# Kernel optimization log

Measured on AMD Instinct MI355X. Metric: run time of the kernel, lower is better.

Reference implementation:

```python
import jax, jax.numpy as jnp
from jax import lax
import numpy as np

B, H, W = 8, 36, 100  # stride-8 feature map of 288x800 input
PAD = 4               # ms_ks // 2 for ms_ks = 9
EPS = 1e-5
FC_IN = 5 * (800 // 16) * (288 // 16)  # 4500


def setup_inputs() -> dict:
    key = jax.random.key(0)
    ks = jax.random.split(key, 12)
    r = lambda k, s, sc: jax.random.normal(k, s, jnp.float32) * sc
    return {
        "x": jax.random.normal(ks[0], (B, 512, H, W), jnp.float32),
        "w1a": r(ks[1], (1024, 512, 3, 3), 0.02),
        "bn1_g": jnp.ones(1024, jnp.float32), "bn1_b": jnp.zeros(1024, jnp.float32),
        "bn1_m": jnp.zeros(1024, jnp.float32), "bn1_v": jnp.ones(1024, jnp.float32),
        "w1b": r(ks[2], (128, 1024, 1, 1), 0.03),
        "bn2_g": jnp.ones(128, jnp.float32), "bn2_b": jnp.zeros(128, jnp.float32),
        "bn2_m": jnp.zeros(128, jnp.float32), "bn2_v": jnp.ones(128, jnp.float32),
        "w_ud": r(ks[3], (128, 128, 9), 0.02),
        "w_du": r(ks[4], (128, 128, 9), 0.02),
        "w_lr": r(ks[5], (128, 128, 9), 0.02),
        "w_rl": r(ks[6], (128, 128, 9), 0.02),
        "w2": r(ks[7], (5, 128, 1, 1), 0.05), "b2": jnp.zeros(5, jnp.float32),
        "fc1_w": r(ks[8], (128, FC_IN), 0.02), "fc1_b": jnp.zeros(128, jnp.float32),
        "fc2_w": r(ks[9], (4, 128), 0.05), "fc2_b": jnp.zeros(4, jnp.float32),
    }


def bn(x, g, b, m, v):
    s = (g / jnp.sqrt(v + EPS))
    return x * s[None, :, None, None] + (b - m * s)[None, :, None, None]


def conv2d(x, w, padding, dilation=(1, 1)):
    return lax.conv_general_dilated(x, w, (1, 1), padding, rhs_dilation=dilation,
                                    dimension_numbers=("NCHW", "OIHW", "NCHW"))


def conv1d(x, w):  # x [B,C,L], w [O,I,K]
    return lax.conv_general_dilated(x, w, (1,), [(PAD, PAD)],
                                    dimension_numbers=("NCH", "OIH", "NCH"))


def message_pass(x, w, axis, reverse):
    # x [B,C,H,W]; scan over `axis`, 1D conv along the other spatial dim
    xs = jnp.moveaxis(x, axis, 0)  # [L, B, C, other]
    if reverse:
        xs = xs[::-1]

    def step(prev, cur):
        new = cur + jax.nn.relu(conv1d(prev, w))
        return new, new

    first = xs[0]
    _, rest = lax.scan(step, first, xs[1:])
    out = jnp.concatenate([first[None], rest], axis=0)
    if reverse:
        out = out[::-1]
    return jnp.moveaxis(out, 0, axis)


def upsample_bilinear_ac(x, scale):
    # align_corners=True bilinear, NCHW
    b, c, h, w = x.shape
    ho, wo = h * scale, w * scale

    def grid(n_in, n_out):
        pos = jnp.arange(n_out, dtype=x.dtype) * ((n_in - 1) / (n_out - 1))
        i0 = jnp.clip(jnp.floor(pos).astype(jnp.int32), 0, n_in - 2)
        return i0, pos - i0.astype(x.dtype)

    i0, fh = grid(h, ho)
    j0, fw = grid(w, wo)
    xh = x[:, :, i0, :] * (1 - fh)[None, None, :, None] + x[:, :, i0 + 1, :] * fh[None, None, :, None]
    return xh[:, :, :, j0] * (1 - fw)[None, None, None, :] + xh[:, :, :, j0 + 1] * fw[None, None, None, :]


def reference(x, w1a, bn1_g, bn1_b, bn1_m, bn1_v, w1b, bn2_g, bn2_b, bn2_m, bn2_v,
              w_ud, w_du, w_lr, w_rl, w2, b2, fc1_w, fc1_b, fc2_w, fc2_b):
    # layer1: dilated 3x3 (pad=4, dil=4) -> BN -> ReLU -> 1x1 -> BN -> ReLU
    h = jax.nn.relu(bn(conv2d(x, w1a, [(4, 4), (4, 4)], dilation=(4, 4)), bn1_g, bn1_b, bn1_m, bn1_v))
    h = jax.nn.relu(bn(conv2d(h, w1b, [(0, 0), (0, 0)]), bn2_g, bn2_b, bn2_m, bn2_v))
    # message passing: up-down, down-up (vertical), left-right, right-left (horizontal)
    h = message_pass(h, w_ud, axis=2, reverse=False)
    h = message_pass(h, w_du, axis=2, reverse=True)
    h = message_pass(h, w_lr, axis=3, reverse=False)
    h = message_pass(h, w_rl, axis=3, reverse=True)
    # layer2 (Dropout2d is identity at eval): 1x1 conv -> 5 channels
    h = conv2d(h, w2, [(0, 0), (0, 0)]) + b2[None, :, None, None]
    seg_pred = upsample_bilinear_ac(h, 8)  # [B,5,288,800]
    # layer3: softmax over channels, then AvgPool2d(2,2)
    p = jax.nn.softmax(h, axis=1)
    b_, c_, hh, ww = p.shape
    p = p.reshape(b_, c_, hh // 2, 2, ww // 2, 2).mean(axis=(3, 5))
    # fc: flatten -> 128 -> ReLU -> 4 -> Sigmoid
    f = p.reshape(b_, -1)
    f = jax.nn.relu(f @ fc1_w.T + fc1_b)
    exist_pred = jax.nn.sigmoid(f @ fc2_w.T + fc2_b)
    return seg_pred, exist_pred
```

## Files before the change

kernel.cpp:

```cpp
#include <hip/hip_runtime.h>
#include <hip/hip_bf16.h>
#include <stdint.h>

typedef __bf16 bf16;
typedef bf16 bf16x8 __attribute__((ext_vector_type(8)));
typedef bf16 bf16x4 __attribute__((ext_vector_type(4)));
typedef float f32x4 __attribute__((ext_vector_type(4)));

#define NB 8
#define NH 36
#define NW 100
#define YS 44
#define XSZ 108
#define PIX 28800

#define AS1 __attribute__((address_space(1)))
#define AS3 __attribute__((address_space(3)))

__device__ __forceinline__ void g2l16(const bf16* g, bf16* l) {
    __builtin_amdgcn_global_load_lds((const AS1 void*)g, (AS3 void*)l, 16, 0, 0);
}

static constexpr size_t OFF_XP = 0;
static constexpr size_t SZ_XP  = (size_t)NB*YS*XSZ*512*2;
static constexpr size_t OFF_HP = OFF_XP + SZ_XP;
static constexpr size_t SZ_HP  = (size_t)NB*YS*XSZ*128*2;
static constexpr size_t OFF_A1 = OFF_HP + SZ_HP;
static constexpr size_t SZ_A1  = (size_t)1024*4608*2;
static constexpr size_t OFF_A2 = OFF_A1 + SZ_A1;
static constexpr size_t SZ_A2  = (size_t)128*1024*2;
static constexpr size_t OFF_AW = OFF_A2 + SZ_A2;
static constexpr size_t SZ_AW  = (size_t)4*9*128*128*2;
static constexpr size_t OFF_H1 = OFF_AW + SZ_AW;
static constexpr size_t SZ_H1  = (size_t)PIX*1024*2;
static constexpr size_t OFF_S1 = OFF_H1 + SZ_H1;
static constexpr size_t OFF_T1 = OFF_S1 + 4096;
static constexpr size_t OFF_S2 = OFF_T1 + 4096;
static constexpr size_t OFF_T2 = OFF_S2 + 512;
static constexpr size_t OFF_H5 = OFF_T2 + 512;
static constexpr size_t SZ_H5  = (size_t)NB*5*3600*4;
static constexpr size_t OFF_P  = OFF_H5 + SZ_H5;
static constexpr size_t OFF_F  = OFF_P + SZ_H5;
static constexpr size_t OFF_G  = OFF_F + 144128;

__global__ __launch_bounds__(256) void zero_k(uint4* __restrict__ p, int n) {
    int i = blockIdx.x * 256 + threadIdx.x;
    if (i < n) p[i] = uint4{0u, 0u, 0u, 0u};
}

__global__ __launch_bounds__(256) void prep_x(const float* __restrict__ x, bf16* __restrict__ xp) {
    int bid = blockIdx.x;
    int xc = bid & 3;  int r = bid >> 2;
    int cc = r & 15;   r >>= 4;
    int yo = r % 36;   int b = r / 36;
    int ci0 = cc * 32, xo0 = xc * 32;
    int wdt = 100 - xo0; if (wdt > 32) wdt = 32;
    __shared__ bf16 T[32 * 33];
    int t = threadIdx.x;
    int cl = t >> 5, xl = t & 31;
    if (xl < wdt) {
#pragma unroll
        for (int i = 0; i < 4; i++) {
            int ci = ci0 + cl + 8 * i;
            T[(cl + 8 * i) * 33 + xl] = (bf16)x[((size_t)(b * 512 + ci) * 36 + yo) * 100 + xo0 + xl];
        }
    }
    __syncthreads();
    if (t < 128) {
        int xo2 = t >> 2, oct = t & 3;
        if (xo2 < wdt) {
            bf16x8 vv;
#pragma unroll
            for (int j = 0; j < 8; j++) vv[j] = T[(oct * 8 + j) * 33 + xo2];
            *(bf16x8*)(xp + ((size_t)((b * YS + yo + 4) * XSZ) + xo0 + xo2 + 4) * 512 + ci0 + oct * 8) = vv;
        }
    }
}

__global__ __launch_bounds__(256) void prep_w1a(const float* __restrict__ w, bf16* __restrict__ A) {
    int co = blockIdx.x;
    __shared__ bf16 Wl[4608];
    const float* src = w + (size_t)co * 4608;
    for (int v = threadIdx.x; v < 4608; v += 256) Wl[v] = (bf16)src[v];
    __syncthreads();
    bf16* dst = A + (size_t)co * 4608;
    for (int v = threadIdx.x; v < 4608; v += 256) {
        int rr = v >> 9, ci = v & 511;
        dst[v] = Wl[ci * 9 + rr];
    }
}

__global__ __launch_bounds__(256) void prep_w1b(const float* __restrict__ w, bf16* __restrict__ A) {
    int i = blockIdx.x * 256 + threadIdx.x;
    if (i < 131072) A[i] = (bf16)w[i];
}

__global__ __launch_bounds__(256) void prep_msg(const float* __restrict__ w0, const float* __restrict__ w1,
                                                const float* __restrict__ w2m, const float* __restrict__ w3,
                                                bf16* __restrict__ Aw) {
    int idx = blockIdx.x * 256 + threadIdx.x;
    if (idx >= 4 * 147456) return;
    int w = idx / 147456, r = idx % 147456;
    int t9 = r / 16384, r2 = r % 16384;
    int co = r2 >> 7, ci = r2 & 127;
    const float* s = (w == 0) ? w0 : (w == 1) ? w1 : (w == 2) ? w2m : w3;
    Aw[idx] = (bf16)s[(co * 128 + ci) * 9 + t9];
}

__global__ __launch_bounds__(256) void prep_bn(const float* g1, const float* b1, const float* m1, const float* v1,
                                               const float* g2, const float* b2i, const float* m2, const float* v2,
                                               float* s1, float* t1, float* s2, float* t2) {
    int i = blockIdx.x * 256 + threadIdx.x;
    if (i < 1024) {
        float s = g1[i] / sqrtf(v1[i] + 1e-5f);
        s1[i] = s; t1[i] = b1[i] - m1[i] * s;
    } else if (i < 1152) {
        int c = i - 1024;
        float s = g2[c] / sqrtf(v2[c] + 1e-5f);
        s2[c] = s; t2[c] = b2i[c] - m2[c] * s;
    }
}

__device__ __forceinline__ void c1_koff(int ch, int& k0, int& xoff) {
    int ky = ch / 48, rem = ch - ky * 48;
    int kx = rem >> 4, c0 = (rem & 15) << 5;
    k0 = (ky * 3 + kx) * 512 + c0;
    xoff = (ky * XSZ + kx) * 2048 + c0;
}

__device__ __forceinline__ bf16x8 lds_frag(const bf16* S, int row, int q) {
    return *(const bf16x8*)(S + row * 32 + (((q ^ (row >> 1)) & 3) * 8));
}

__global__ __launch_bounds__(256) void conv1_gemm(const bf16* __restrict__ A, const bf16* __restrict__ xp,
                                                  const float* __restrict__ s1, const float* __restrict__ t1,
                                                  bf16* __restrict__ h1) {
    __shared__ __align__(16) bf16 SH[17408];
    bf16* As = SH;
    bf16* Bs = SH + 4096;
    const int t = threadIdx.x;
    const int pt = blockIdx.x, ct = blockIdx.y;
    const int co0 = ct * 128, p0 = pt * 128;
    const int wid = t >> 6, lane = t & 63;

    int aOff[2], bOff[2], ldsOff[2];
#pragma unroll
    for (int j = 0; j < 2; j++) {
        int p = wid * 128 + j * 64 + lane;
        int row = p >> 2;
        int oc = (p & 3) ^ ((p >> 3) & 3);
        aOff[j] = (co0 + row) * 4608 + oc * 8;
        int px = p0 + row;
        int b = px / 3600, rr = px % 3600;
        int y = rr / 100, xx = rr % 100;
        bOff[j] = ((b * YS + y) * XSZ + xx) * 512 + oc * 8;
        ldsOff[j] = (wid * 128 + j * 64) * 8;
    }

    const int mbase = (wid & 1) * 64, nbase = (wid >> 1) * 64;
    const int l15 = lane & 15, q = lane >> 4;

    f32x4 acc[4][4];
#pragma unroll
    for (int i = 0; i < 4; i++)
#pragma unroll
        for (int j = 0; j < 4; j++) acc[i][j] = f32x4{0.f, 0.f, 0.f, 0.f};

    for (int ch = 0; ch < 144; ch++) {
        int k0, xoff;
        c1_koff(ch, k0, xoff);
        __syncthreads();
#pragma unroll
        for (int j = 0; j < 2; j++) {
            g2l16(A + aOff[j] + k0, As + ldsOff[j]);
            g2l16(xp + bOff[j] + xoff, Bs + ldsOff[j]);
        }
        __syncthreads();
        bf16x8 af[4], bfv[4];
#pragma unroll
        for (int mt = 0; mt < 4; mt++) af[mt] = lds_frag(As, mbase + mt * 16 + l15, q);
#pragma unroll
        for (int nt = 0; nt < 4; nt++) bfv[nt] = lds_frag(Bs, nbase + nt * 16 + l15, q);
#pragma unroll
        for (int mt = 0; mt < 4; mt++)
#pragma unroll
            for (int nt = 0; nt < 4; nt++)
                acc[mt][nt] = __builtin_amdgcn_mfma_f32_16x16x32_bf16(af[mt], bfv[nt], acc[mt][nt], 0, 0, 0);
    }

    __syncthreads();
#pragma unroll
    for (int mt = 0; mt < 4; mt++) {
        int co = co0 + mbase + mt * 16 + q * 4;
        f32x4 sc = *(const f32x4*)(s1 + co);
        f32x4 tc = *(const f32x4*)(t1 + co);
#pragma unroll
        for (int nt = 0; nt < 4; nt++) {
            int pxl = nbase + nt * 16 + l15;
            bf16x4 o;
#pragma unroll
            for (int r = 0; r < 4; r++) {
                float v = acc[mt][nt][r] * sc[r] + tc[r];
                o[r] = (bf16)(v > 0.f ? v : 0.f);
            }
            *(bf16x4*)(SH + pxl * 136 + mbase + mt * 16 + q * 4) = o;
        }
    }
    __syncthreads();
#pragma unroll
    for (int i = 0; i < 8; i++) {
        int v = t + 256 * i;
        int pxl = v >> 4, c16 = v & 15;
        *(uint4*)(h1 + (size_t)(p0 + pxl) * 1024 + co0 + c16 * 8) = *(const uint4*)(SH + pxl * 136 + c16 * 8);
    }
}

__global__ __launch_bounds__(256) void conv2_gemm(const bf16* __restrict__ A2, const bf16* __restrict__ h1,
                                                  const float* __restrict__ s2, const float* __restrict__ t2,
                                                  bf16* __restrict__ hp) {
    __shared__ __align__(16) bf16 SH[17408];
    bf16* As = SH;
    bf16* Bs = SH + 4096;
    const int t = threadIdx.x;
    const int p0 = blockIdx.x * 128;
    const int wid = t >> 6, lane = t & 63;

    int aOff[2], bOff[2], ldsOff[2];
#pragma unroll
    for (int j = 0; j < 2; j++) {
        int p = wid * 128 + j * 64 + lane;
        int row = p >> 2;
        int oc = (p & 3) ^ ((p >> 3) & 3);
        aOff[j] = row * 1024 + oc * 8;
        bOff[j] = (p0 + row) * 1024 + oc * 8;
        ldsOff[j] = (wid * 128 + j * 64) * 8;
    }
    const int mbase = (wid & 1) * 64, nbase = (wid >> 1) * 64;
    const int l15 = lane & 15, q = lane >> 4;

    f32x4 acc[4][4];
#pragma unroll
    for (int i = 0; i < 4; i++)
#pragma unroll
        for (int j = 0; j < 4; j++) acc[i][j] = f32x4{0.f, 0.f, 0.f, 0.f};

    for (int ch = 0; ch < 32; ch++) {
        int k0 = ch * 32;
        __syncthreads();
#pragma unroll
        for (int j = 0; j < 2; j++) {
            g2l16(A2 + aOff[j] + k0, As + ldsOff[j]);
            g2l16(h1 + bOff[j] + k0, Bs + ldsOff[j]);
        }
        __syncthreads();
        bf16x8 af[4], bfv[4];
#pragma unroll
        for (int mt = 0; mt < 4; mt++) af[mt] = lds_frag(As, mbase + mt * 16 + l15, q);
#pragma unroll
        for (int nt = 0; nt < 4; nt++) bfv[nt] = lds_frag(Bs, nbase + nt * 16 + l15, q);
#pragma unroll
        for (int mt = 0; mt < 4; mt++)
#pragma unroll
            for (int nt = 0; nt < 4; nt++)
                acc[mt][nt] = __builtin_amdgcn_mfma_f32_16x16x32_bf16(af[mt], bfv[nt], acc[mt][nt], 0, 0, 0);
    }

    __syncthreads();
#pragma unroll
    for (int mt = 0; mt < 4; mt++) {
        int co = mbase + mt * 16 + q * 4;
        f32x4 sc = *(const f32x4*)(s2 + co);
        f32x4 tc = *(const f32x4*)(t2 + co);
#pragma unroll
        for (int nt = 0; nt < 4; nt++) {
            int pxl = nbase + nt * 16 + l15;
            bf16x4 o;
#pragma unroll
            for (int r = 0; r < 4; r++) {
                float v = acc[mt][nt][r] * sc[r] + tc[r];
                o[r] = (bf16)(v > 0.f ? v : 0.f);
            }
            *(bf16x4*)(SH + pxl * 136 + co) = o;
        }
    }
    __syncthreads();
#pragma unroll
    for (int i = 0; i < 8; i++) {
        int v = t + 256 * i;
        int pxl = v >> 4, c16 = v & 15;
        int p = p0 + pxl;
        int b = p / 3600, rr = p % 3600;
        int y = rr / 100, xx = rr % 100;
        *(uint4*)(hp + (size_t)((b * YS + y + 4) * XSZ + xx + 4) * 128 + c16 * 8) = *(const uint4*)(SH + pxl * 136 + c16 * 8);
    }
}

__device__ __forceinline__ bf16x8 awfrag(const bf16* __restrict__ Aw, int ch, int mt, int l15, int q) {
    int t9 = ch >> 2, c0 = (ch & 3) << 5;
    return *(const bf16x8*)(Aw + (size_t)((t9 * 128 + mt * 16 + l15) << 7) + c0 + q * 8);
}

template <int AX, int RV>
__device__ void msg_phase(const bf16* __restrict__ Aw, bf16* __restrict__ hpb,
                          bf16* __restrict__ Rb, int t) {
    constexpr int STEPS = (AX == 2) ? NH : NW;
    constexpr int NLIM  = (AX == 2) ? NW : NH;
    constexpr int NT    = (AX == 2) ? 7 : 3;
    constexpr int LINE  = (AX == 2) ? XSZ : YS;
    const int wid = t >> 6, lane = t & 63, l15 = lane & 15, q = lane >> 4;

    bf16x8 a[36][2];
#pragma unroll
    for (int ch = 0; ch < 36; ch++)
#pragma unroll
        for (int mt = 0; mt < 2; mt++)
            a[ch][mt] = awfrag(Aw, ch, wid * 2 + mt, l15, q);

    __threadfence();

    if (AX == 2) {
        int ys0 = RV ? 39 : 4;
        for (int v = t; v < LINE * 16; v += 256) {
            int xs = v >> 4, oct = v & 15;
            *(uint4*)(Rb + xs * 136 + oct * 8) = *(const uint4*)(hpb + ((size_t)ys0 * XSZ + xs) * 128 + oct * 8);
        }
    } else {
        int xs0 = RV ? 103 : 4;
        for (int v = t; v < LINE * 16; v += 256) {
            int ys = v >> 4, oct = v & 15;
            *(uint4*)(Rb + ys * 136 + oct * 8) = *(const uint4*)(hpb + ((size_t)ys * XSZ + xs0) * 128 + oct * 8);
        }
    }
    __syncthreads();

    for (int s = 1; s < STEPS; s++) {
        int pos = RV ? (STEPS - 1 - s) : s;

        f32x4 acc[2][NT];
#pragma unroll
        for (int mt = 0; mt < 2; mt++)
#pragma unroll
            for (int nt = 0; nt < NT; nt++) acc[mt][nt] = f32x4{0.f, 0.f, 0.f, 0.f};

#pragma unroll
        for (int ch = 0; ch < 36; ch++) {
            int t9 = ch >> 2, c0 = (ch & 3) << 5;
            bf16x8 bfv[NT];
#pragma unroll
            for (int nt = 0; nt < NT; nt++)
                bfv[nt] = *(const bf16x8*)(Rb + (nt * 16 + l15 + t9) * 136 + c0 + q * 8);
#pragma unroll
            for (int mt = 0; mt < 2; mt++)
#pragma unroll
                for (int nt = 0; nt < NT; nt++)
                    acc[mt][nt] = __builtin_amdgcn_mfma_f32_16x16x32_bf16(a[ch][mt], bfv[nt], acc[mt][nt], 0, 0, 0);
        }
        __syncthreads();

        bf16x4 curv[2][NT];
#pragma unroll
        for (int mt = 0; mt < 2; mt++) {
            int co = wid * 32 + mt * 16 + q * 4;
#pragma unroll
            for (int nt = 0; nt < NT; nt++) {
                int n = nt * 16 + l15;
                if (n < NLIM) {
                    int g = (AX == 2) ? ((pos + 4) * XSZ + (n + 4)) * 128 + co
                                      : ((n + 4) * XSZ + (pos + 4)) * 128 + co;
                    curv[mt][nt] = *(const bf16x4*)(hpb + g);
                }
            }
        }
#pragma unroll
        for (int mt = 0; mt < 2; mt++) {
            int co = wid * 32 + mt * 16 + q * 4;
#pragma unroll
            for (int nt = 0; nt < NT; nt++) {
                int n = nt * 16 + l15;
                if (n < NLIM) {
                    int g = (AX == 2) ? ((pos + 4) * XSZ + (n + 4)) * 128 + co
                                      : ((n + 4) * XSZ + (pos + 4)) * 128 + co;
                    bf16x4 o;
#pragma unroll
                    for (int r = 0; r < 4; r++) {
                        float v = acc[mt][nt][r];
                        v = v > 0.f ? v : 0.f;
                        o[r] = (bf16)((float)curv[mt][nt][r] + v);
                    }
                    *(bf16x4*)(hpb + g) = o;
                    *(bf16x4*)(Rb + (n + 4) * 136 + co) = o;
                }
            }
        }
        __syncthreads();
    }
}

__global__ __launch_bounds__(256, 1) void msg_fused(const bf16* __restrict__ Aw, bf16* __restrict__ hp) {
    __shared__ __align__(16) bf16 Rb[120 * 136];
    const int b = blockIdx.x;
    const int t = threadIdx.x;
    bf16* hpb = hp + (size_t)b * YS * XSZ * 128;

    msg_phase<2, 0>(Aw + 0 * 147456, hpb, Rb, t);
    __syncthreads();
    msg_phase<2, 1>(Aw + 1 * 147456, hpb, Rb, t);
    __syncthreads();
    msg_phase<3, 0>(Aw + 2 * 147456, hpb, Rb, t);
    __syncthreads();
    msg_phase<3, 1>(Aw + 3 * 147456, hpb, Rb, t);
}

__global__ __launch_bounds__(256) void conv3_softmax(const bf16* __restrict__ hp, const float* __restrict__ w2,
                                                     const float* __restrict__ b2, float* __restrict__ h5,
                                                     float* __restrict__ Pp) {
    int idx = blockIdx.x * 256 + threadIdx.x;
    if (idx >= PIX) return;
    int b = idx / 3600, rr = idx % 3600;
    int y = rr / 100, xx = rr % 100;
    const bf16* src = hp + ((size_t)(b * YS + y + 4) * XSZ + xx + 4) * 128;
    float a[5] = {b2[0], b2[1], b2[2], b2[3], b2[4]};
    for (int c8 = 0; c8 < 128; c8 += 8) {
        bf16x8 hv = *(const bf16x8*)(src + c8);
#pragma unroll
        for (int j = 0; j < 8; j++) {
            float hf = (float)hv[j];
            int c = c8 + j;
#pragma unroll
            for (int o = 0; o < 5; o++) a[o] += hf * w2[o * 128 + c];
        }
    }
    float mx = a[0];
#pragma unroll
    for (int o = 1; o < 5; o++) mx = a[o] > mx ? a[o] : mx;
    float e[5], sum = 0.f;
#pragma unroll
    for (int o = 0; o < 5; o++) { e[o] = expf(a[o] - mx); sum += e[o]; }
    float inv = 1.f / sum;
#pragma unroll
    for (int o = 0; o < 5; o++) {
        h5[(size_t)(b * 5 + o) * 3600 + rr] = a[o];
        Pp[(size_t)(b * 5 + o) * 3600 + rr] = e[o] * inv;
    }
}

__global__ __launch_bounds__(256) void pool_k(const float* __restrict__ Pp, float* __restrict__ F) {
    int idx = blockIdx.x * 256 + threadIdx.x;
    if (idx >= 36000) return;
    int xxp = idx % 50, r = idx / 50;
    int yyp = r % 18, bj = r / 18;
    int b = bj / 5, j = bj % 5;
    const float* Pb = Pp + (size_t)bj * 3600;
    float v = 0.25f * (Pb[(2 * yyp) * 100 + 2 * xxp] + Pb[(2 * yyp) * 100 + 2 * xxp + 1] +
                       Pb[(2 * yyp + 1) * 100 + 2 * xxp] + Pb[(2 * yyp + 1) * 100 + 2 * xxp + 1]);
    F[(size_t)b * 4500 + j * 900 + yyp * 50 + xxp] = v;
}

__global__ __launch_bounds__(64) void fc1_k(const float* __restrict__ F, const float* __restrict__ w,
                                            const float* __restrict__ bias, float* __restrict__ G) {
    int co = blockIdx.x;
    int lane = threadIdx.x;
    const float* wr = w + (size_t)co * 4500;
    float a[8] = {0.f, 0.f, 0.f, 0.f, 0.f, 0.f, 0.f, 0.f};
    for (int k = lane; k < 4500; k += 64) {
        float wv = wr[k];
#pragma unroll
        for (int b = 0; b < 8; b++) a[b] += wv * F[b * 4500 + k];
    }
#pragma unroll
    for (int b = 0; b < 8; b++) {
        float r = a[b];
        for (int off = 32; off; off >>= 1) r += __shfl_down(r, off);
        if (lane == 0) {
            float v = r + bias[co];
            G[b * 128 + co] = v > 0.f ? v : 0.f;
        }
    }
}

__global__ __launch_bounds__(64) void fc2_k(const float* __restrict__ G, const float* __restrict__ w,
                                            const float* __restrict__ bias, float* __restrict__ out) {
    int t = threadIdx.x;
    if (t >= 32) return;
    int b = t >> 2, j = t & 3;
    float a = bias[j];
    for (int c = 0; c < 128; c++) a += G[b * 128 + c] * w[j * 128 + c];
    out[9216000 + b * 4 + j] = 1.f / (1.f + expf(-a));
}

__global__ __launch_bounds__(256) void upsample_k(const float* __restrict__ h5, float* __restrict__ out) {
    int idx = blockIdx.x * 256 + threadIdx.x;
    if (idx >= 2304000) return;
    int xq = idx % 200, r = idx / 200;
    int yo = r % 288, bj = r / 288;
    const float* src = h5 + (size_t)bj * 3600;
    float py = yo * (35.0f / 287.0f);
    int i0 = (int)py; if (i0 > 34) i0 = 34;
    float fh = py - (float)i0;
    const float* r0 = src + i0 * 100;
    const float* r1 = r0 + 100;
    float4 o;
    float res[4];
#pragma unroll
    for (int e = 0; e < 4; e++) {
        int xo = xq * 4 + e;
        float px = xo * (99.0f / 799.0f);
        int j0 = (int)px; if (j0 > 98) j0 = 98;
        float fw = px - (float)j0;
        float aa = r0[j0] * (1.f - fh) + r1[j0] * fh;
        float bb = r0[j0 + 1] * (1.f - fh) + r1[j0 + 1] * fh;
        res[e] = aa * (1.f - fw) + bb * fw;
    }
    o.x = res[0]; o.y = res[1]; o.z = res[2]; o.w = res[3];
    *(float4*)(out + (size_t)idx * 4) = o;
}

extern "C" void kernel_launch(void* const* d_in, const int* in_sizes, int n_in,
                              void* d_out, int out_size, void* d_ws, size_t ws_size,
                              hipStream_t stream) {
    (void)in_sizes; (void)n_in; (void)out_size; (void)ws_size;
    const float* x    = (const float*)d_in[0];
    const float* w1a  = (const float*)d_in[1];
    const float* bn1g = (const float*)d_in[2];
    const float* bn1b = (const float*)d_in[3];
    const float* bn1m = (const float*)d_in[4];
    const float* bn1v = (const float*)d_in[5];
    const float* w1b  = (const float*)d_in[6];
    const float* bn2g = (const float*)d_in[7];
    const float* bn2b = (const float*)d_in[8];
    const float* bn2m = (const float*)d_in[9];
    const float* bn2v = (const float*)d_in[10];
    const float* wud  = (const float*)d_in[11];
    const float* wdu  = (const float*)d_in[12];
    const float* wlr  = (const float*)d_in[13];
    const float* wrl  = (const float*)d_in[14];
    const float* w2   = (const float*)d_in[15];
    const float* b2   = (const float*)d_in[16];
    const float* fc1w = (const float*)d_in[17];
    const float* fc1b = (const float*)d_in[18];
    const float* fc2w = (const float*)d_in[19];
    const float* fc2b = (const float*)d_in[20];
    float* out = (float*)d_out;
    char* ws = (char*)d_ws;
    bf16* xp = (bf16*)(ws + OFF_XP);
    bf16* hp = (bf16*)(ws + OFF_HP);
    bf16* A1 = (bf16*)(ws + OFF_A1);
    bf16* A2 = (bf16*)(ws + OFF_A2);
    bf16* Aw = (bf16*)(ws + OFF_AW);
    bf16* h1 = (bf16*)(ws + OFF_H1);
    float* s1 = (float*)(ws + OFF_S1);
    float* t1 = (float*)(ws + OFF_T1);
    float* s2 = (float*)(ws + OFF_S2);
    float* t2 = (float*)(ws + OFF_T2);
    float* h5 = (float*)(ws + OFF_H5);
    float* Pp = (float*)(ws + OFF_P);
    float* Ff = (float*)(ws + OFF_F);
    float* Gg = (float*)(ws + OFF_G);

    int nzero = (int)((SZ_XP + SZ_HP) / 16);
    zero_k<<<(nzero + 255) / 256, 256, 0, stream>>>((uint4*)ws, nzero);
    prep_x<<<18432, 256, 0, stream>>>(x, xp);
    prep_w1a<<<1024, 256, 0, stream>>>(w1a, A1);
    prep_w1b<<<512, 256, 0, stream>>>(w1b, A2);
    prep_msg<<<2304, 256, 0, stream>>>(wud, wdu, wlr, wrl, Aw);
    prep_bn<<<5, 256, 0, stream>>>(bn1g, bn1b, bn1m, bn1v, bn2g, bn2b, bn2m, bn2v, s1, t1, s2, t2);

    conv1_gemm<<<dim3(225, 8), 256, 0, stream>>>(A1, xp, s1, t1, h1);
    conv2_gemm<<<225, 256, 0, stream>>>(A2, h1, s2, t2, hp);

    msg_fused<<<NB, 256, 0, stream>>>(Aw, hp);

    conv3_softmax<<<113, 256, 0, stream>>>(hp, w2, b2, h5, Pp);
    pool_k<<<141, 256, 0, stream>>>(Pp, Ff);
    fc1_k<<<128, 64, 0, stream>>>(Ff, fc1w, fc1b, Gg);
    fc2_k<<<1, 64, 0, stream>>>(Gg, fc2w, fc2b, out);
    upsample_k<<<9000, 256, 0, stream>>>(h5, out);
}
```

Before: 2.406 ms.

## Split message passing across 64 blocks with per-batch global atomic barriers

The sequential message-passing kernel previously ran one block per batch image, each computing all 128 output channels. It now launches 8 blocks per image, each owning a 16-channel slice. Every step reloads the previous line from global memory into LDS and synchronises the 8 blocks with a spin-wait atomic counter barrier. This spreads the serial recurrence over more CUs, at the cost of a global barrier and global reload per step, and it relies on all 64 blocks being co-resident.

```diff
diff --git a/kernel.cpp b/kernel.cpp
--- a/kernel.cpp
+++ b/kernel.cpp
@@ -42,6 +42,7 @@
 static constexpr size_t OFF_P  = OFF_H5 + SZ_H5;
 static constexpr size_t OFF_F  = OFF_P + SZ_H5;
 static constexpr size_t OFF_G  = OFF_F + 144128;
+static constexpr size_t OFF_BAR = OFF_G + 4096;
 
 __global__ __launch_bounds__(256) void zero_k(uint4* __restrict__ p, int n) {
     int i = blockIdx.x * 256 + threadIdx.x;
@@ -109,7 +110,8 @@
 
 __global__ __launch_bounds__(256) void prep_bn(const float* g1, const float* b1, const float* m1, const float* v1,
                                                const float* g2, const float* b2i, const float* m2, const float* v2,
-                                               float* s1, float* t1, float* s2, float* t2) {
+                                               float* s1, float* t1, float* s2, float* t2,
+                                               unsigned* bar) {
     int i = blockIdx.x * 256 + threadIdx.x;
     if (i < 1024) {
         float s = g1[i] / sqrtf(v1[i] + 1e-5f);
@@ -118,6 +120,8 @@
         int c = i - 1024;
         float s = g2[c] / sqrtf(v2[c] + 1e-5f);
         s2[c] = s; t2[c] = b2i[c] - m2[c] * s;
+    } else if (i < 1160) {
+        bar[i - 1152] = 0u;
     }
 }
 
@@ -295,120 +299,109 @@
     }
 }
 
-__device__ __forceinline__ bf16x8 awfrag(const bf16* __restrict__ Aw, int ch, int mt, int l15, int q) {
+__device__ __forceinline__ bf16x8 awfrag2(const bf16* __restrict__ Aw, int ch, int cs, int l15, int q) {
     int t9 = ch >> 2, c0 = (ch & 3) << 5;
-    return *(const bf16x8*)(Aw + (size_t)((t9 * 128 + mt * 16 + l15) << 7) + c0 + q * 8);
+    return *(const bf16x8*)(Aw + (size_t)((t9 * 128 + cs * 16 + l15) << 7) + c0 + q * 8);
+}
+
+__device__ __forceinline__ void gbar(unsigned* ctr, int target) {
+    __syncthreads();
+    if (threadIdx.x == 0) {
+        __hip_atomic_fetch_add(ctr, 1u, __ATOMIC_RELEASE, __HIP_MEMORY_SCOPE_AGENT);
+        while ((int)__hip_atomic_load(ctr, __ATOMIC_ACQUIRE, __HIP_MEMORY_SCOPE_AGENT) < target)
+            __builtin_amdgcn_s_sleep(2);
+    }
+    __syncthreads();
 }
 
 template <int AX, int RV>
-__device__ void msg_phase(const bf16* __restrict__ Aw, bf16* __restrict__ hpb,
-                          bf16* __restrict__ Rb, int t) {
+__device__ void msg_phase2(const bf16* __restrict__ Aw, bf16* __restrict__ hpb,
+                           bf16* __restrict__ Rb, unsigned* ctr, int cs, int& ep) {
     constexpr int STEPS = (AX == 2) ? NH : NW;
     constexpr int NLIM  = (AX == 2) ? NW : NH;
-    constexpr int NT    = (AX == 2) ? 7 : 3;
-    constexpr int LINE  = (AX == 2) ? XSZ : YS;
-    const int wid = t >> 6, lane = t & 63, l15 = lane & 15, q = lane >> 4;
-
-    bf16x8 a[36][2];
-#pragma unroll
-    for (int ch = 0; ch < 36; ch++)
-#pragma unroll
-        for (int mt = 0; mt < 2; mt++)
-            a[ch][mt] = awfrag(Aw, ch, wid * 2 + mt, l15, q);
-
-    __threadfence();
-
-    if (AX == 2) {
-        int ys0 = RV ? 39 : 4;
-        for (int v = t; v < LINE * 16; v += 256) {
-            int xs = v >> 4, oct = v & 15;
-            *(uint4*)(Rb + xs * 136 + oct * 8) = *(const uint4*)(hpb + ((size_t)ys0 * XSZ + xs) * 128 + oct * 8);
-        }
-    } else {
-        int xs0 = RV ? 103 : 4;
-        for (int v = t; v < LINE * 16; v += 256) {
-            int ys = v >> 4, oct = v & 15;
-            *(uint4*)(Rb + ys * 136 + oct * 8) = *(const uint4*)(hpb + ((size_t)ys * XSZ + xs0) * 128 + oct * 8);
-        }
-    }
-    __syncthreads();
+    constexpr int NTW   = (AX == 2) ? 2 : 1;
+    const int t = threadIdx.x, wid = t >> 6, lane = t & 63, l15 = lane & 15, q = lane >> 4;
+
+    bf16x8 a[36];
+#pragma unroll
+    for (int ch = 0; ch < 36; ch++) a[ch] = awfrag2(Aw, ch, cs, l15, q);
+
+    const int nb0 = (AX == 2) ? wid * 32 : wid * 16;
+    bool act[NTW];
+#pragma unroll
+    for (int i = 0; i < NTW; i++) act[i] = (nb0 + i * 16) < NLIM;
+    const int co = cs * 16 + q * 4;
 
     for (int s = 1; s < STEPS; s++) {
         int pos = RV ? (STEPS - 1 - s) : s;
-
-        f32x4 acc[2][NT];
-#pragma unroll
-        for (int mt = 0; mt < 2; mt++)
-#pragma unroll
-            for (int nt = 0; nt < NT; nt++) acc[mt][nt] = f32x4{0.f, 0.f, 0.f, 0.f};
-
+        int prv = RV ? pos + 1 : pos - 1;
+
+        if (AX == 2) {
+            const bf16* src = hpb + (size_t)(prv + 4) * XSZ * 128;
+            for (int v = t; v < 108 * 16; v += 256) {
+                int px = v >> 4, c = (v & 15) * 8;
+                *(uint4*)(Rb + px * 136 + c) = *(const uint4*)(src + px * 128 + c);
+            }
+        } else {
+            const bf16* src = hpb + (size_t)(prv + 4) * 128;
+            for (int v = t; v < 44 * 16; v += 256) {
+                int ys = v >> 4, c = (v & 15) * 8;
+                *(uint4*)(Rb + ys * 136 + c) = *(const uint4*)(src + (size_t)ys * XSZ * 128 + c);
+            }
+        }
+        __syncthreads();
+
+        f32x4 acc[NTW];
+#pragma unroll
+        for (int i = 0; i < NTW; i++) acc[i] = f32x4{0.f, 0.f, 0.f, 0.f};
 #pragma unroll
         for (int ch = 0; ch < 36; ch++) {
             int t9 = ch >> 2, c0 = (ch & 3) << 5;
-            bf16x8 bfv[NT];
-#pragma unroll
-            for (int nt = 0; nt < NT; nt++)
-                bfv[nt] = *(const bf16x8*)(Rb + (nt * 16 + l15 + t9) * 136 + c0 + q * 8);
-#pragma unroll
-            for (int mt = 0; mt < 2; mt++)
-#pragma unroll
-                for (int nt = 0; nt < NT; nt++)
-                    acc[mt][nt] = __builtin_amdgcn_mfma_f32_16x16x32_bf16(a[ch][mt], bfv[nt], acc[mt][nt], 0, 0, 0);
-        }
-        __syncthreads();
-
-        bf16x4 curv[2][NT];
-#pragma unroll
-        for (int mt = 0; mt < 2; mt++) {
-            int co = wid * 32 + mt * 16 + q * 4;
-#pragma unroll
-            for (int nt = 0; nt < NT; nt++) {
-                int n = nt * 16 + l15;
-                if (n < NLIM) {
-                    int g = (AX == 2) ? ((pos + 4) * XSZ + (n + 4)) * 128 + co
-                                      : ((n + 4) * XSZ + (pos + 4)) * 128 + co;
-                    curv[mt][nt] = *(const bf16x4*)(hpb + g);
+#pragma unroll
+            for (int i = 0; i < NTW; i++) {
+                if (act[i]) {
+                    bf16x8 bfv = *(const bf16x8*)(Rb + (nb0 + i * 16 + l15 + t9) * 136 + c0 + q * 8);
+                    acc[i] = __builtin_amdgcn_mfma_f32_16x16x32_bf16(a[ch], bfv, acc[i], 0, 0, 0);
                 }
             }
         }
-#pragma unroll
-        for (int mt = 0; mt < 2; mt++) {
-            int co = wid * 32 + mt * 16 + q * 4;
-#pragma unroll
-            for (int nt = 0; nt < NT; nt++) {
-                int n = nt * 16 + l15;
+
+#pragma unroll
+        for (int i = 0; i < NTW; i++) {
+            if (act[i]) {
+                int n = nb0 + i * 16 + l15;
                 if (n < NLIM) {
-                    int g = (AX == 2) ? ((pos + 4) * XSZ + (n + 4)) * 128 + co
-                                      : ((n + 4) * XSZ + (pos + 4)) * 128 + co;
+                    size_t g = (AX == 2) ? ((size_t)(pos + 4) * XSZ + (n + 4)) * 128 + co
+                                         : ((size_t)(n + 4) * XSZ + (pos + 4)) * 128 + co;
+                    bf16x4 cur = *(const bf16x4*)(hpb + g);
                     bf16x4 o;
 #pragma unroll
                     for (int r = 0; r < 4; r++) {
-                        float v = acc[mt][nt][r];
+                        float v = acc[i][r];
                         v = v > 0.f ? v : 0.f;
-                        o[r] = (bf16)((float)curv[mt][nt][r] + v);
+                        o[r] = (bf16)((float)cur[r] + v);
                     }
                     *(bf16x4*)(hpb + g) = o;
-                    *(bf16x4*)(Rb + (n + 4) * 136 + co) = o;
                 }
             }
         }
-        __syncthreads();
-    }
-}
-
-__global__ __launch_bounds__(256, 1) void msg_fused(const bf16* __restrict__ Aw, bf16* __restrict__ hp) {
+        ep++;
+        gbar(ctr, 8 * ep);
+    }
+}
+
+__global__ __launch_bounds__(256, 1) void msg_fused(const bf16* __restrict__ Aw, bf16* __restrict__ hp,
+                                                    unsigned* __restrict__ bar) {
     __shared__ __align__(16) bf16 Rb[120 * 136];
-    const int b = blockIdx.x;
-    const int t = threadIdx.x;
-    bf16* hpb = hp + (size_t)b * YS * XSZ * 128;
-
-    msg_phase<2, 0>(Aw + 0 * 147456, hpb, Rb, t);
-    __syncthreads();
-    msg_phase<2, 1>(Aw + 1 * 147456, hpb, Rb, t);
-    __syncthreads();
-    msg_phase<3, 0>(Aw + 2 * 147456, hpb, Rb, t);
-    __syncthreads();
-    msg_phase<3, 1>(Aw + 3 * 147456, hpb, Rb, t);
+    const int batch = blockIdx.x & 7;
+    const int cs = blockIdx.x >> 3;
+    bf16* hpb = hp + (size_t)batch * YS * XSZ * 128;
+    unsigned* ctr = bar + batch;
+    int ep = 0;
+    msg_phase2<2, 0>(Aw + 0 * 147456, hpb, Rb, ctr, cs, ep);
+    msg_phase2<2, 1>(Aw + 1 * 147456, hpb, Rb, ctr, cs, ep);
+    msg_phase2<3, 0>(Aw + 2 * 147456, hpb, Rb, ctr, cs, ep);
+    msg_phase2<3, 1>(Aw + 3 * 147456, hpb, Rb, ctr, cs, ep);
 }
 
 __global__ __launch_bounds__(256) void conv3_softmax(const bf16* __restrict__ hp, const float* __restrict__ w2,
@@ -556,6 +549,7 @@
     float* Pp = (float*)(ws + OFF_P);
     float* Ff = (float*)(ws + OFF_F);
     float* Gg = (float*)(ws + OFF_G);
+    unsigned* bar = (unsigned*)(ws + OFF_BAR);
 
     int nzero = (int)((SZ_XP + SZ_HP) / 16);
     zero_k<<<(nzero + 255) / 256, 256, 0, stream>>>((uint4*)ws, nzero);
@@ -563,12 +557,12 @@
     prep_w1a<<<1024, 256, 0, stream>>>(w1a, A1);
     prep_w1b<<<512, 256, 0, stream>>>(w1b, A2);
     prep_msg<<<2304, 256, 0, stream>>>(wud, wdu, wlr, wrl, Aw);
-    prep_bn<<<5, 256, 0, stream>>>(bn1g, bn1b, bn1m, bn1v, bn2g, bn2b, bn2m, bn2v, s1, t1, s2, t2);
+    prep_bn<<<5, 256, 0, stream>>>(bn1g, bn1b, bn1m, bn1v, bn2g, bn2b, bn2m, bn2v, s1, t1, s2, t2, bar);
 
     conv1_gemm<<<dim3(225, 8), 256, 0, stream>>>(A1, xp, s1, t1, h1);
     conv2_gemm<<<225, 256, 0, stream>>>(A2, h1, s2, t2, hp);
 
-    msg_fused<<<NB, 256, 0, stream>>>(Aw, hp);
+    msg_fused<<<64, 256, 0, stream>>>(Aw, hp, bar);
 
     conv3_softmax<<<113, 256, 0, stream>>>(hp, w2, b2, h5, Pp);
     pool_k<<<141, 256, 0, stream>>>(Pp, Ff);
```

Result: faster. 2.121 ms (-11.9%).
